# Kernel tuning notes

Measured on AMD Instinct MI355X. Metric: run time of the kernel, lower is better.

The kernel has to match this reference:

```python
import jax, jax.numpy as jnp
import numpy as np

HIDDEN = 1024
INTER = 4096

def setup_inputs() -> dict:
    key = jax.random.key(0)
    k1, k2, k3, k4, k5 = jax.random.split(key, 5)
    hidden_states = jax.random.normal(k1, (4, 2048, HIDDEN), dtype=jnp.float32)
    # Linear params: W stored pre-transposed as [in, out], matching W = dense.weight.t()
    W1 = jax.random.normal(k2, (HIDDEN, INTER), dtype=jnp.float32) * (1.0 / np.sqrt(HIDDEN))
    b1 = jax.random.normal(k3, (INTER,), dtype=jnp.float32) * 0.02
    W2 = jax.random.normal(k4, (INTER, HIDDEN), dtype=jnp.float32) * (1.0 / np.sqrt(INTER))
    b2 = jax.random.normal(k5, (HIDDEN,), dtype=jnp.float32) * 0.02
    return {"hidden_states": hidden_states, "W1": W1, "b1": b1, "W2": W2, "b2": b2}

def reference(hidden_states, W1, b1, W2, b2):
    # Tiled loops in the original are exactly a dense 2-layer MLP with ReLU.
    h = jax.nn.relu(jnp.einsum('bsh,hi->bsi', hidden_states, W1) + b1)
    return jnp.einsum('bsi,ih->bsh', h, W2) + b2
```

## Files before the change

kernel.cpp:

```cpp
#include <hip/hip_runtime.h>
#include <cstddef>

typedef short short8 __attribute__((ext_vector_type(8)));
typedef unsigned short ushort8 __attribute__((ext_vector_type(8)));
typedef float f32x4 __attribute__((ext_vector_type(4)));

#define AS1(p) ((const __attribute__((address_space(1))) void*)(p))
#define AS3(p) ((__attribute__((address_space(3))) void*)(p))

__device__ __forceinline__ unsigned short f2bf(float f) {
  unsigned int u = __builtin_bit_cast(unsigned int, f);
  u += 0x7FFFu + ((u >> 16) & 1u);
  return (unsigned short)(u >> 16);
}

__device__ __forceinline__ void gload_lds16(const void* g, void* l) {
  __builtin_amdgcn_global_load_lds(AS1(g), AS3(l), 16, 0, 0);
}

__global__ void cvt_f32_bf16(const float* __restrict__ in,
                             unsigned short* __restrict__ out, int n4) {
  int i = blockIdx.x * blockDim.x + threadIdx.x;
  if (i >= n4) return;
  float4 v = *reinterpret_cast<const float4*>(in + (size_t)i * 4);
  ushort4 o;
  o.x = f2bf(v.x); o.y = f2bf(v.y); o.z = f2bf(v.z); o.w = f2bf(v.w);
  *reinterpret_cast<ushort4*>(out + (size_t)i * 4) = o;
}

__global__ void transpose_cvt(const float* __restrict__ in,
                              unsigned short* __restrict__ out,
                              int Kd, int Nd) {
  __shared__ float tile[32][33];
  const int n0 = blockIdx.x * 32;
  const int k0 = blockIdx.y * 32;
  const int tx = threadIdx.x;
  const int ty = threadIdx.y;
#pragma unroll
  for (int i = 0; i < 4; ++i)
    tile[ty + i * 8][tx] = in[(size_t)(k0 + ty + i * 8) * Nd + n0 + tx];
  __syncthreads();
#pragma unroll
  for (int i = 0; i < 4; ++i)
    out[(size_t)(n0 + ty + i * 8) * Kd + k0 + tx] = f2bf(tile[tx][ty + i * 8]);
}

template <int A_F32, int RELU_BF16_OUT>
__global__ __launch_bounds__(256, 2)
void gemm_bf16(const void* __restrict__ Ap, int lda,
               const unsigned short* __restrict__ B, int ldb,
               const float* __restrict__ bias,
               void* __restrict__ C, int ldc,
               int K, int beta) {
  __shared__ char lds[32768];
  char* const As = lds;
  char* const Bs = lds + 16384;

  const int tid  = threadIdx.x;
  const int lane = tid & 63;
  const int w    = tid >> 6;
  const int wm   = w >> 1;
  const int wn   = w & 1;
  const int m0   = blockIdx.y * 128;
  const int n0   = blockIdx.x * 128;

  f32x4 acc[4][4];
#pragma unroll
  for (int i = 0; i < 4; ++i)
#pragma unroll
    for (int j = 0; j < 4; ++j)
      acc[i][j] = (f32x4){0.f, 0.f, 0.f, 0.f};

  int srow[4], scol[4], sbase[4];
#pragma unroll
  for (int j = 0; j < 4; ++j) {
    const int stored  = (j * 256 + tid) * 16;
    const int natural = stored ^ (((stored >> 7) & 7) << 4);
    srow[j]  = natural >> 7;
    scol[j]  = (natural & 127) >> 1;
    sbase[j] = (j * 256 + (tid & 192)) * 16;
  }

  size_t agofs[4];
  int ast[4];
  if (A_F32) {
#pragma unroll
    for (int p = 0; p < 4; ++p) {
      const int idx = p * 256 + tid;
      const int r   = idx >> 3;
      const int kbe = (idx & 7) * 8;
      agofs[p] = (size_t)(m0 + r) * lda + kbe;
      const int nat = r * 128 + kbe * 2;
      ast[p] = nat ^ (((nat >> 7) & 7) << 4);
    }
  }

  const int nsteps = K >> 6;
  for (int ks = 0; ks < nsteps; ++ks) {
    const int k0 = ks << 6;
    if (A_F32) {
      const float* Af = (const float*)Ap;
#pragma unroll
      for (int p = 0; p < 4; ++p) {
        const float* s = Af + agofs[p] + k0;
        float4 x0 = *reinterpret_cast<const float4*>(s);
        float4 x1 = *reinterpret_cast<const float4*>(s + 4);
        ushort8 v;
        v[0] = f2bf(x0.x); v[1] = f2bf(x0.y); v[2] = f2bf(x0.z); v[3] = f2bf(x0.w);
        v[4] = f2bf(x1.x); v[5] = f2bf(x1.y); v[6] = f2bf(x1.z); v[7] = f2bf(x1.w);
        *reinterpret_cast<ushort8*>(As + ast[p]) = v;
      }
    } else {
      const unsigned short* Ab = (const unsigned short*)Ap;
#pragma unroll
      for (int j = 0; j < 4; ++j)
        gload_lds16(Ab + (size_t)(m0 + srow[j]) * lda + (k0 + scol[j]),
                    As + sbase[j]);
    }
#pragma unroll
    for (int j = 0; j < 4; ++j)
      gload_lds16(B + (size_t)(n0 + srow[j]) * ldb + (k0 + scol[j]),
                  Bs + sbase[j]);
    __syncthreads();

#pragma unroll
    for (int kk = 0; kk < 2; ++kk) {
      const int kb = kk * 64 + (lane >> 4) * 16;
      short8 af[4], bfv[4];
#pragma unroll
      for (int mi = 0; mi < 4; ++mi) {
        int nat = (wm * 64 + mi * 16 + (lane & 15)) * 128 + kb;
        int st  = nat ^ (((nat >> 7) & 7) << 4);
        af[mi] = *reinterpret_cast<const short8*>(As + st);
      }
#pragma unroll
      for (int ni = 0; ni < 4; ++ni) {
        int nat = (wn * 64 + ni * 16 + (lane & 15)) * 128 + kb;
        int st  = nat ^ (((nat >> 7) & 7) << 4);
        bfv[ni] = *reinterpret_cast<const short8*>(Bs + st);
      }
#pragma unroll
      for (int mi = 0; mi < 4; ++mi)
#pragma unroll
        for (int ni = 0; ni < 4; ++ni)
          acc[mi][ni] = __builtin_amdgcn_mfma_f32_16x16x32_bf16(
              af[mi], bfv[ni], acc[mi][ni], 0, 0, 0);
    }
    __syncthreads();
  }

  const int row0 = m0 + wm * 64 + (lane >> 4) * 4;
  const int col0 = n0 + wn * 64 + (lane & 15);
#pragma unroll
  for (int ni = 0; ni < 4; ++ni) {
    const int c = col0 + ni * 16;
    const float bv = beta ? 0.f : bias[c];
#pragma unroll
    for (int mi = 0; mi < 4; ++mi) {
#pragma unroll
      for (int r = 0; r < 4; ++r) {
        const size_t idx = (size_t)(row0 + mi * 16 + r) * ldc + c;
        float v = acc[mi][ni][r] + bv;
        if (RELU_BF16_OUT) {
          v = v > 0.f ? v : 0.f;
          ((unsigned short*)C)[idx] = f2bf(v);
        } else {
          if (beta) v += ((float*)C)[idx];
          ((float*)C)[idx] = v;
        }
      }
    }
  }
}

extern "C" void kernel_launch(void* const* d_in, const int* in_sizes, int n_in,
                              void* d_out, int out_size, void* d_ws, size_t ws_size,
                              hipStream_t stream) {
  const float* X  = (const float*)d_in[0];
  const float* W1 = (const float*)d_in[1];
  const float* b1 = (const float*)d_in[2];
  const float* W2 = (const float*)d_in[3];
  const float* b2 = (const float*)d_in[4];
  float* out = (float*)d_out;

  const int M = 8192, H = 1024, I = 4096;
  const size_t MB = 1024 * 1024;

  char* ws = (char*)d_ws;
  unsigned short* W1t = (unsigned short*)ws;
  unsigned short* W2t = (unsigned short*)(ws + 8 * MB);

  int Ic;
  int useXbf;
  unsigned short* Xbf = nullptr;
  unsigned short* Hc;
  if (ws_size >= 80 * MB) {
    Ic = 4096; useXbf = 1;
    Xbf = (unsigned short*)((char*)d_out + 16 * MB);
    Hc  = (unsigned short*)(ws + 16 * MB);
  } else if (ws_size >= 64 * MB) {
    Ic = 2048; useXbf = 1;
    Xbf = (unsigned short*)(ws + 16 * MB);
    Hc  = (unsigned short*)(ws + 32 * MB);
  } else if (ws_size >= 48 * MB) {
    Ic = 1024; useXbf = 1;
    Xbf = (unsigned short*)(ws + 16 * MB);
    Hc  = (unsigned short*)(ws + 32 * MB);
  } else if (ws_size >= 32 * MB) {
    Ic = 1024; useXbf = 0;
    Hc  = (unsigned short*)(ws + 16 * MB);
  } else if (ws_size >= 24 * MB) {
    Ic = 512;  useXbf = 0;
    Hc  = (unsigned short*)(ws + 16 * MB);
  } else if (ws_size >= 20 * MB) {
    Ic = 256;  useXbf = 0;
    Hc  = (unsigned short*)(ws + 16 * MB);
  } else {
    Ic = 128;  useXbf = 0;
    Hc  = (unsigned short*)(ws + 16 * MB);
  }

  transpose_cvt<<<dim3(I / 32, H / 32), dim3(32, 8), 0, stream>>>(W1, W1t, H, I);
  transpose_cvt<<<dim3(H / 32, I / 32), dim3(32, 8), 0, stream>>>(W2, W2t, I, H);
  if (useXbf) {
    int n4 = (M * H) / 4;
    cvt_f32_bf16<<<(n4 + 255) / 256, 256, 0, stream>>>(X, Xbf, n4);
  }

  const int nch = I / Ic;
  for (int c = 0; c < nch; ++c) {
    const int i0 = c * Ic;
    if (useXbf)
      gemm_bf16<0, 1><<<dim3(Ic / 128, M / 128), 256, 0, stream>>>(
          Xbf, H, W1t + (size_t)i0 * H, H, b1 + i0, Hc, Ic, H, 0);
    else
      gemm_bf16<1, 1><<<dim3(Ic / 128, M / 128), 256, 0, stream>>>(
          X, H, W1t + (size_t)i0 * H, H, b1 + i0, Hc, Ic, H, 0);
    gemm_bf16<0, 0><<<dim3(H / 128, M / 128), 256, 0, stream>>>(
        Hc, Ic, W2t + i0, I, b2, out, H, Ic, c > 0);
  }
}
```

Before: 168.4 us.

## Add 256-row double-buffered 8-wave GEMM with XCD-aware block remap

Adds a new GEMM kernel with 512 threads and 256xBN tiles. It double-buffers A and B in LDS over 128-wide K steps and splits each step into eight phases, so global-to-LDS loads overlap MFMA work. Barriers, explicit waitcnts and setprio are placed by hand, and block IDs are remapped across the eight XCDs. When the workspace is large, both GEMMs now use this kernel, which aims at higher MFMA utilisation and better reuse. The cost is 128 KB of LDS, which limits occupancy, and fragile hand-tuned synchronisation.

```diff
diff --git a/kernel.cpp b/kernel.cpp
--- a/kernel.cpp
+++ b/kernel.cpp
@@ -43,6 +43,162 @@
 #pragma unroll
   for (int i = 0; i < 4; ++i)
     out[(size_t)(n0 + ty + i * 8) * Kd + k0 + tx] = f2bf(tile[tx][ty + i * 8]);
+}
+
+#define PH(ABUF, BBUF, H, KK, STAGE, WAITC)                                    \
+  {                                                                            \
+    if ((H) == 0) {                                                            \
+      _Pragma("unroll")                                                        \
+      for (int ni = 0; ni < NB; ++ni)                                          \
+        bfr[ni] = *reinterpret_cast<const short8*>((BBUF) + bread[ni][KK]);    \
+    }                                                                          \
+    short8 afr[4];                                                             \
+    _Pragma("unroll")                                                          \
+    for (int m2 = 0; m2 < 4; ++m2)                                             \
+      afr[m2] = *reinterpret_cast<const short8*>((ABUF) + aread[(H)*4+m2][KK]);\
+    STAGE;                                                                     \
+    __builtin_amdgcn_s_barrier();                                              \
+    asm volatile("s_waitcnt lgkmcnt(0)" ::: "memory");                         \
+    __builtin_amdgcn_sched_barrier(0);                                         \
+    __builtin_amdgcn_s_setprio(1);                                             \
+    _Pragma("unroll")                                                          \
+    for (int m2 = 0; m2 < 4; ++m2) {                                           \
+      _Pragma("unroll")                                                        \
+      for (int ni = 0; ni < NB; ++ni)                                          \
+        acc[(H)*4+m2][ni] = __builtin_amdgcn_mfma_f32_16x16x32_bf16(           \
+            afr[m2], bfr[ni], acc[(H)*4+m2][ni], 0, 0, 0);                     \
+    }                                                                          \
+    __builtin_amdgcn_s_setprio(0);                                             \
+    WAITC;                                                                     \
+    __builtin_amdgcn_s_barrier();                                              \
+  }
+
+template <int BN, int RELU_BF16_OUT>
+__global__ __launch_bounds__(512, 2)
+void gemm8p(const unsigned short* __restrict__ A, int lda,
+            const unsigned short* __restrict__ Bp, int ldb,
+            const float* __restrict__ bias,
+            void* __restrict__ C, int ldc, int K, int nbx) {
+  constexpr int PWN     = BN / 4;
+  constexpr int NB      = PWN / 16;
+  constexpr int LOADS_B = BN / 128;
+  constexpr int BHROWS  = BN / 2;
+  constexpr int BHSZ    = BHROWS * 128;
+  extern __shared__ char lds[];
+  char* const A0b = lds;
+  char* const A1b = lds + 32768;
+  char* const B0b = lds + 65536;
+  char* const B1b = lds + 65536 + 2 * BHSZ;
+
+  const int tid  = threadIdx.x;
+  const int lane = tid & 63;
+  const int wid  = tid >> 6;
+  const int wm   = wid >> 2;
+  const int wn   = wid & 3;
+
+  const int cpx     = gridDim.x >> 3;
+  const int logical = (blockIdx.x & 7) * cpx + (blockIdx.x >> 3);
+  const int bx = logical % nbx;
+  const int by = logical / nbx;
+  const int m0 = by * 256;
+  const int n0 = bx * BN;
+
+  f32x4 acc[8][NB];
+#pragma unroll
+  for (int i = 0; i < 8; ++i)
+#pragma unroll
+    for (int j = 0; j < NB; ++j)
+      acc[i][j] = (f32x4){0.f, 0.f, 0.f, 0.f};
+
+  size_t aofs0, aofs1, bofs0, bofs1 = 0;
+  {
+    int sr = tid * 16, nat = sr ^ (((sr >> 7) & 7) << 4);
+    aofs0 = (size_t)(m0 + (nat >> 7)) * lda + ((nat & 127) >> 1);
+    bofs0 = (size_t)(n0 + (nat >> 7)) * ldb + ((nat & 127) >> 1);
+    sr = (512 + tid) * 16; nat = sr ^ (((sr >> 7) & 7) << 4);
+    aofs1 = (size_t)(m0 + (nat >> 7)) * lda + ((nat & 127) >> 1);
+    if (LOADS_B == 2)
+      bofs1 = (size_t)(n0 + (nat >> 7)) * ldb + ((nat & 127) >> 1);
+  }
+  const int dst0 = (tid & 448) * 16;
+  const int dst1 = dst0 + 8192;
+
+  auto stA = [&](char* ab, int half, int kel) {
+    gload_lds16(A + aofs0 + (size_t)half * 128 * lda + kel, ab + half * 16384 + dst0);
+    gload_lds16(A + aofs1 + (size_t)half * 128 * lda + kel, ab + half * 16384 + dst1);
+  };
+  auto stB = [&](char* bb, int half, int kel) {
+    gload_lds16(Bp + bofs0 + (size_t)half * BHROWS * ldb + kel, bb + half * BHSZ + dst0);
+    if constexpr (LOADS_B == 2)
+      gload_lds16(Bp + bofs1 + (size_t)half * BHROWS * ldb + kel, bb + half * BHSZ + dst1);
+  };
+  auto waitLB = [&]() {
+    if constexpr (LOADS_B == 2) asm volatile("s_waitcnt vmcnt(2)" ::: "memory");
+    else                        asm volatile("s_waitcnt vmcnt(1)" ::: "memory");
+  };
+
+  int aread[8][2], bread[NB][2];
+#pragma unroll
+  for (int mi = 0; mi < 8; ++mi)
+#pragma unroll
+    for (int kk = 0; kk < 2; ++kk) {
+      int nat = (wm * 128 + mi * 16 + (lane & 15)) * 128 + kk * 64 + (lane >> 4) * 16;
+      aread[mi][kk] = nat ^ (((nat >> 7) & 7) << 4);
+    }
+#pragma unroll
+  for (int ni = 0; ni < NB; ++ni)
+#pragma unroll
+    for (int kk = 0; kk < 2; ++kk) {
+      int nat = (wn * PWN + ni * 16 + (lane & 15)) * 128 + kk * 64 + (lane >> 4) * 16;
+      bread[ni][kk] = nat ^ (((nat >> 7) & 7) << 4);
+    }
+
+  stB(B0b, 0, 0);
+  stB(B0b, 1, 0);
+  stA(A0b, 0, 0);
+  stA(A0b, 1, 0);
+  stB(B1b, 0, 64);
+  waitLB();
+  __builtin_amdgcn_s_barrier();
+
+  const int niter = K >> 7;
+  for (int it = 0; it < niter; ++it) {
+    const bool last = (it == niter - 1);
+    const int kb = it << 7;
+    short8 bfr[NB];
+    PH(A0b, B0b, 0, 0, stB(B1b, 1, kb + 64), ((void)0));
+    PH(A0b, B0b, 1, 0, stA(A1b, 0, kb + 64), ((void)0));
+    PH(A0b, B0b, 0, 1, stA(A1b, 1, kb + 64), ((void)0));
+    PH(A0b, B0b, 1, 1, { if (!last) stB(B0b, 0, kb + 128); },
+       { if (last) { asm volatile("s_waitcnt vmcnt(0)" ::: "memory"); } else waitLB(); });
+    PH(A1b, B1b, 0, 0, { if (!last) stB(B0b, 1, kb + 128); }, ((void)0));
+    PH(A1b, B1b, 1, 0, { if (!last) stA(A0b, 0, kb + 128); }, ((void)0));
+    PH(A1b, B1b, 0, 1, { if (!last) stA(A0b, 1, kb + 128); }, ((void)0));
+    PH(A1b, B1b, 1, 1, { if (!last) stB(B1b, 0, kb + 192); },
+       { if (!last) waitLB(); });
+  }
+
+  const int row0 = m0 + wm * 128 + (lane >> 4) * 4;
+  const int col0 = n0 + wn * PWN + (lane & 15);
+#pragma unroll
+  for (int ni = 0; ni < NB; ++ni) {
+    const int c = col0 + ni * 16;
+    const float bv = bias[c];
+#pragma unroll
+    for (int mi = 0; mi < 8; ++mi) {
+#pragma unroll
+      for (int r = 0; r < 4; ++r) {
+        const size_t idx = (size_t)(row0 + mi * 16 + r) * ldc + c;
+        float v = acc[mi][ni][r] + bv;
+        if (RELU_BF16_OUT) {
+          v = v > 0.f ? v : 0.f;
+          ((unsigned short*)C)[idx] = f2bf(v);
+        } else {
+          ((float*)C)[idx] = v;
+        }
+      }
+    }
+  }
 }
 
 template <int A_F32, int RELU_BF16_OUT>
@@ -190,15 +346,23 @@
   unsigned short* W1t = (unsigned short*)ws;
   unsigned short* W2t = (unsigned short*)(ws + 8 * MB);
 
-  int Ic;
-  int useXbf;
+  transpose_cvt<<<dim3(I / 32, H / 32), dim3(32, 8), 0, stream>>>(W1, W1t, H, I);
+  transpose_cvt<<<dim3(H / 32, I / 32), dim3(32, 8), 0, stream>>>(W2, W2t, I, H);
+
+  if (ws_size >= 80 * MB) {
+    unsigned short* Xbf = (unsigned short*)((char*)d_out + 16 * MB);
+    unsigned short* Hbf = (unsigned short*)(ws + 16 * MB);
+    int n4 = (M * H) / 4;
+    cvt_f32_bf16<<<(n4 + 255) / 256, 256, 0, stream>>>(X, Xbf, n4);
+    gemm8p<256, 1><<<512, 512, 131072, stream>>>(Xbf, H, W1t, H, b1, Hbf, I, H, I / 256);
+    gemm8p<128, 0><<<256, 512, 98304, stream>>>(Hbf, I, W2t, I, b2, out, H, I, H / 128);
+    return;
+  }
+
+  int Ic, useXbf;
   unsigned short* Xbf = nullptr;
   unsigned short* Hc;
-  if (ws_size >= 80 * MB) {
-    Ic = 4096; useXbf = 1;
-    Xbf = (unsigned short*)((char*)d_out + 16 * MB);
-    Hc  = (unsigned short*)(ws + 16 * MB);
-  } else if (ws_size >= 64 * MB) {
+  if (ws_size >= 64 * MB) {
     Ic = 2048; useXbf = 1;
     Xbf = (unsigned short*)(ws + 16 * MB);
     Hc  = (unsigned short*)(ws + 32 * MB);
@@ -220,8 +384,6 @@
     Hc  = (unsigned short*)(ws + 16 * MB);
   }
 
-  transpose_cvt<<<dim3(I / 32, H / 32), dim3(32, 8), 0, stream>>>(W1, W1t, H, I);
-  transpose_cvt<<<dim3(H / 32, I / 32), dim3(32, 8), 0, stream>>>(W2, W2t, I, H);
   if (useXbf) {
     int n4 = (M * H) / 4;
     cvt_f32_bf16<<<(n4 + 255) / 256, 256, 0, stream>>>(X, Xbf, n4);
```

Result: no change. 165.4 us (-1.7%).

## Add 4-stage LDS ring-buffered 256-row GEMM kernel for large-workspace path

Applied to the files above, without the earlier changes.

Introduces a new gemm_ring kernel with 512 threads and 256xBN tiles. It uses a 4-slot LDS ring filled by direct global-to-LDS loads three k-steps ahead, with explicit vmcnt waits, sched barriers and setprio around the MFMA blocks. It also remaps block IDs into XCD-grouped order and uses a new XOR swizzle. The large-workspace path now runs both GEMMs with this kernel, which aims to hide memory latency and raise MFMA utilisation. In exchange it uses much more LDS and registers, and the hand-coded wait counts must match the issue order exactly.

```diff
diff --git a/kernel.cpp b/kernel.cpp
--- a/kernel.cpp
+++ b/kernel.cpp
@@ -16,6 +16,11 @@
 
 __device__ __forceinline__ void gload_lds16(const void* g, void* l) {
   __builtin_amdgcn_global_load_lds(AS1(g), AS3(l), 16, 0, 0);
+}
+
+template <int N>
+__device__ __forceinline__ void vwait() {
+  asm volatile("s_waitcnt vmcnt(%0)" :: "n"(N) : "memory");
 }
 
 __global__ void cvt_f32_bf16(const float* __restrict__ in,
@@ -43,6 +48,146 @@
 #pragma unroll
   for (int i = 0; i < 4; ++i)
     out[(size_t)(n0 + ty + i * 8) * Kd + k0 + tx] = f2bf(tile[tx][ty + i * 8]);
+}
+
+#define TILE_BODY(T, DO_STAGE, STAGE_T)                                        \
+  {                                                                            \
+    char* s = lds + (size_t)((T) & 3) * SLOT;                                  \
+    _Pragma("unroll")                                                          \
+    for (int h = 0; h < NPH; ++h) {                                            \
+      if (h == 0) {                                                            \
+        _Pragma("unroll")                                                      \
+        for (int ni = 0; ni < 4; ++ni)                                         \
+          bfr[ni] = *reinterpret_cast<const short8*>(s + brd[ni]);             \
+      }                                                                        \
+      short8 afr[4];                                                           \
+      _Pragma("unroll")                                                        \
+      for (int m2 = 0; m2 < 4; ++m2)                                           \
+        afr[m2] = *reinterpret_cast<const short8*>(s + ard[h * 4 + m2]);       \
+      if (h == 0 && (DO_STAGE)) stage(STAGE_T);                                \
+      asm volatile("s_waitcnt lgkmcnt(0)" ::: "memory");                       \
+      __builtin_amdgcn_sched_barrier(0);                                       \
+      __builtin_amdgcn_s_setprio(1);                                           \
+      _Pragma("unroll")                                                        \
+      for (int m2 = 0; m2 < 4; ++m2) {                                         \
+        _Pragma("unroll")                                                      \
+        for (int ni = 0; ni < 4; ++ni)                                         \
+          acc[h * 4 + m2][ni] = __builtin_amdgcn_mfma_f32_16x16x32_bf16(       \
+              afr[m2], bfr[ni], acc[h * 4 + m2][ni], 0, 0, 0);                 \
+      }                                                                        \
+      __builtin_amdgcn_s_setprio(0);                                           \
+    }                                                                          \
+  }
+
+#define TILE_END(WN_)                                                          \
+  vwait<WN_>();                                                                \
+  __builtin_amdgcn_s_barrier();                                                \
+  __builtin_amdgcn_sched_barrier(0);
+
+template <int WM, int BN, int RELU_BF16_OUT>
+__global__ __launch_bounds__(512, 2)
+void gemm_ring(const unsigned short* __restrict__ A, int lda,
+               const unsigned short* __restrict__ B, int ldb,
+               const float* __restrict__ bias,
+               void* __restrict__ C, int ldc, int K, int nbx) {
+  constexpr int WN     = 8 / WM;
+  constexpr int MB     = 256 / WM / 16;
+  constexpr int NPH    = MB / 4;
+  constexpr int BUNITS = BN / 128;
+  constexpr int UNITS  = 2 + BUNITS;
+  constexpr int SLOT   = 16384 + BN * 64;
+  extern __shared__ char lds[];
+
+  const int tid  = threadIdx.x;
+  const int lane = tid & 63;
+  const int wid  = tid >> 6;
+  const int wm   = wid / WN;
+  const int wn   = wid % WN;
+
+  const int cpx     = gridDim.x >> 3;
+  const int logical = (blockIdx.x & 7) * cpx + (blockIdx.x >> 3);
+  const int bx = logical % nbx;
+  const int by = logical / nbx;
+  const int m0 = by * 256;
+  const int n0 = bx * BN;
+
+  f32x4 acc[MB][4];
+#pragma unroll
+  for (int i = 0; i < MB; ++i)
+#pragma unroll
+    for (int j = 0; j < 4; ++j)
+      acc[i][j] = (f32x4){0.f, 0.f, 0.f, 0.f};
+
+  const int p    = tid * 16;
+  const int r    = p >> 6;
+  const int smsk = (((r & 3) ^ ((r >> 2) & 3)) << 4);
+  const int kel0 = (((p & 63) ^ smsk) >> 1);
+  size_t aofs0 = (size_t)(m0 + r) * lda + kel0;
+  size_t aofs1 = (size_t)(m0 + 128 + r) * lda + kel0;
+  size_t bofs0 = (size_t)(n0 + r) * ldb + kel0;
+  size_t bofs1 = (BUNITS == 2) ? (size_t)(n0 + 128 + r) * ldb + kel0 : 0;
+  const int ldst = (tid >> 6) * 1024;
+
+  auto stage = [&](int t) {
+    char* s = lds + (size_t)(t & 3) * SLOT;
+    const int kk = t * 32;
+    gload_lds16(A + aofs0 + kk, s + ldst);
+    gload_lds16(A + aofs1 + kk, s + 8192 + ldst);
+    gload_lds16(B + bofs0 + kk, s + 16384 + ldst);
+    if constexpr (BUNITS == 2)
+      gload_lds16(B + bofs1 + kk, s + 24576 + ldst);
+  };
+
+  int ard[MB], brd[4];
+#pragma unroll
+  for (int mi = 0; mi < MB; ++mi) {
+    int nat = (wm * (MB * 16) + mi * 16 + (lane & 15)) * 64 + (lane >> 4) * 16;
+    int rr  = nat >> 6;
+    ard[mi] = nat ^ ((((rr & 3) ^ ((rr >> 2) & 3))) << 4);
+  }
+#pragma unroll
+  for (int ni = 0; ni < 4; ++ni) {
+    int nat = (wn * 64 + ni * 16 + (lane & 15)) * 64 + (lane >> 4) * 16;
+    int rr  = nat >> 6;
+    brd[ni] = 16384 + (nat ^ ((((rr & 3) ^ ((rr >> 2) & 3))) << 4));
+  }
+
+  stage(0); stage(1); stage(2);
+  TILE_END(2 * UNITS);
+
+  const int NT = K >> 5;
+  short8 bfr[4];
+  for (int t = 0; t < NT - 3; ++t) {
+    TILE_BODY(t, true, t + 3);
+    TILE_END(2 * UNITS);
+  }
+  TILE_BODY(NT - 3, false, 0);
+  TILE_END(UNITS);
+  TILE_BODY(NT - 2, false, 0);
+  TILE_END(0);
+  TILE_BODY(NT - 1, false, 0);
+
+  const int row0 = m0 + wm * (MB * 16) + (lane >> 4) * 4;
+  const int col0 = n0 + wn * 64 + (lane & 15);
+#pragma unroll
+  for (int ni = 0; ni < 4; ++ni) {
+    const int c = col0 + ni * 16;
+    const float bv = bias[c];
+#pragma unroll
+    for (int mi = 0; mi < MB; ++mi) {
+#pragma unroll
+      for (int rr = 0; rr < 4; ++rr) {
+        const size_t idx = (size_t)(row0 + mi * 16 + rr) * ldc + c;
+        float v = acc[mi][ni][rr] + bv;
+        if (RELU_BF16_OUT) {
+          v = v > 0.f ? v : 0.f;
+          ((unsigned short*)C)[idx] = f2bf(v);
+        } else {
+          ((float*)C)[idx] = v;
+        }
+      }
+    }
+  }
 }
 
 template <int A_F32, int RELU_BF16_OUT>
@@ -85,13 +230,13 @@
   int ast[4];
   if (A_F32) {
 #pragma unroll
-    for (int p = 0; p < 4; ++p) {
-      const int idx = p * 256 + tid;
-      const int r   = idx >> 3;
+    for (int pq = 0; pq < 4; ++pq) {
+      const int idx = pq * 256 + tid;
+      const int rr  = idx >> 3;
       const int kbe = (idx & 7) * 8;
-      agofs[p] = (size_t)(m0 + r) * lda + kbe;
-      const int nat = r * 128 + kbe * 2;
-      ast[p] = nat ^ (((nat >> 7) & 7) << 4);
+      agofs[pq] = (size_t)(m0 + rr) * lda + kbe;
+      const int nat = rr * 128 + kbe * 2;
+      ast[pq] = nat ^ (((nat >> 7) & 7) << 4);
     }
   }
 
@@ -101,14 +246,14 @@
     if (A_F32) {
       const float* Af = (const float*)Ap;
 #pragma unroll
-      for (int p = 0; p < 4; ++p) {
-        const float* s = Af + agofs[p] + k0;
-        float4 x0 = *reinterpret_cast<const float4*>(s);
-        float4 x1 = *reinterpret_cast<const float4*>(s + 4);
+      for (int pq = 0; pq < 4; ++pq) {
+        const float* sp = Af + agofs[pq] + k0;
+        float4 x0 = *reinterpret_cast<const float4*>(sp);
+        float4 x1 = *reinterpret_cast<const float4*>(sp + 4);
         ushort8 v;
         v[0] = f2bf(x0.x); v[1] = f2bf(x0.y); v[2] = f2bf(x0.z); v[3] = f2bf(x0.w);
         v[4] = f2bf(x1.x); v[5] = f2bf(x1.y); v[6] = f2bf(x1.z); v[7] = f2bf(x1.w);
-        *reinterpret_cast<ushort8*>(As + ast[p]) = v;
+        *reinterpret_cast<ushort8*>(As + ast[pq]) = v;
       }
     } else {
       const unsigned short* Ab = (const unsigned short*)Ap;
@@ -158,9 +303,9 @@
 #pragma unroll
     for (int mi = 0; mi < 4; ++mi) {
 #pragma unroll
-      for (int r = 0; r < 4; ++r) {
-        const size_t idx = (size_t)(row0 + mi * 16 + r) * ldc + c;
-        float v = acc[mi][ni][r] + bv;
+      for (int rr = 0; rr < 4; ++rr) {
+        const size_t idx = (size_t)(row0 + mi * 16 + rr) * ldc + c;
+        float v = acc[mi][ni][rr] + bv;
         if (RELU_BF16_OUT) {
           v = v > 0.f ? v : 0.f;
           ((unsigned short*)C)[idx] = f2bf(v);
@@ -190,15 +335,25 @@
   unsigned short* W1t = (unsigned short*)ws;
   unsigned short* W2t = (unsigned short*)(ws + 8 * MB);
 
-  int Ic;
-  int useXbf;
+  transpose_cvt<<<dim3(I / 32, H / 32), dim3(32, 8), 0, stream>>>(W1, W1t, H, I);
+  transpose_cvt<<<dim3(H / 32, I / 32), dim3(32, 8), 0, stream>>>(W2, W2t, I, H);
+
+  if (ws_size >= 80 * MB) {
+    unsigned short* Xbf = (unsigned short*)((char*)d_out + 16 * MB);
+    unsigned short* Hbf = (unsigned short*)(ws + 16 * MB);
+    int n4 = (M * H) / 4;
+    cvt_f32_bf16<<<(n4 + 255) / 256, 256, 0, stream>>>(X, Xbf, n4);
+    gemm_ring<2, 256, 1><<<512, 512, 131072, stream>>>(
+        Xbf, H, W1t, H, b1, Hbf, I, H, I / 256);
+    gemm_ring<4, 128, 0><<<256, 512, 98304, stream>>>(
+        Hbf, I, W2t, I, b2, out, H, I, H / 128);
+    return;
+  }
+
+  int Ic, useXbf;
   unsigned short* Xbf = nullptr;
   unsigned short* Hc;
-  if (ws_size >= 80 * MB) {
-    Ic = 4096; useXbf = 1;
-    Xbf = (unsigned short*)((char*)d_out + 16 * MB);
-    Hc  = (unsigned short*)(ws + 16 * MB);
-  } else if (ws_size >= 64 * MB) {
+  if (ws_size >= 64 * MB) {
     Ic = 2048; useXbf = 1;
     Xbf = (unsigned short*)(ws + 16 * MB);
     Hc  = (unsigned short*)(ws + 32 * MB);
@@ -220,8 +375,6 @@
     Hc  = (unsigned short*)(ws + 16 * MB);
   }
 
-  transpose_cvt<<<dim3(I / 32, H / 32), dim3(32, 8), 0, stream>>>(W1, W1t, H, I);
-  transpose_cvt<<<dim3(H / 32, I / 32), dim3(32, 8), 0, stream>>>(W2, W2t, I, H);
   if (useXbf) {
     int n4 = (M * H) / 4;
     cvt_f32_bf16<<<(n4 + 255) / 256, 256, 0, stream>>>(X, Xbf, n4);
```

Result: slower. 172.9 us (+2.7%).

## Use narrower N tile for second GEMM, XCD-aware block remap, raise occupancy

Applied to the files above, without the earlier changes.

Templates the GEMM on the N tile width and uses a 128x64 tile for the second GEMM, which doubles that grid to 1024 blocks and improves load balance across CUs. Blocks are launched on a 1D grid and remapped so consecutive logical tiles land on the same XCD (blockIdx mod 8), aiming at better L2 reuse. Launch bounds rise to 4 waves per SIMD to raise occupancy, which risks register pressure. The narrower tile lowers B reuse per block and adds more A reloads.

```diff
diff --git a/kernel.cpp b/kernel.cpp
--- a/kernel.cpp
+++ b/kernel.cpp
@@ -45,14 +45,16 @@
     out[(size_t)(n0 + ty + i * 8) * Kd + k0 + tx] = f2bf(tile[tx][ty + i * 8]);
 }
 
-template <int A_F32, int RELU_BF16_OUT>
-__global__ __launch_bounds__(256, 2)
+template <int A_F32, int BN, int RELU_BF16_OUT>
+__global__ __launch_bounds__(256, 4)
 void gemm_bf16(const void* __restrict__ Ap, int lda,
                const unsigned short* __restrict__ B, int ldb,
                const float* __restrict__ bias,
                void* __restrict__ C, int ldc,
-               int K, int beta) {
-  __shared__ char lds[32768];
+               int K, int beta, int nbx) {
+  constexpr int BUNITS = BN / 32;
+  constexpr int NB     = BN / 32;
+  __shared__ char lds[16384 + BN * 128];
   char* const As = lds;
   char* const Bs = lds + 16384;
 
@@ -61,14 +63,17 @@
   const int w    = tid >> 6;
   const int wm   = w >> 1;
   const int wn   = w & 1;
-  const int m0   = blockIdx.y * 128;
-  const int n0   = blockIdx.x * 128;
-
-  f32x4 acc[4][4];
+
+  const int cpx     = gridDim.x >> 3;
+  const int logical = (blockIdx.x & 7) * cpx + (blockIdx.x >> 3);
+  const int m0 = (logical / nbx) * 128;
+  const int n0 = (logical % nbx) * BN;
+
+  f32x4 acc[4][NB];
 #pragma unroll
   for (int i = 0; i < 4; ++i)
 #pragma unroll
-    for (int j = 0; j < 4; ++j)
+    for (int j = 0; j < NB; ++j)
       acc[i][j] = (f32x4){0.f, 0.f, 0.f, 0.f};
 
   int srow[4], scol[4], sbase[4];
@@ -118,7 +123,7 @@
                     As + sbase[j]);
     }
 #pragma unroll
-    for (int j = 0; j < 4; ++j)
+    for (int j = 0; j < BUNITS; ++j)
       gload_lds16(B + (size_t)(n0 + srow[j]) * ldb + (k0 + scol[j]),
                   Bs + sbase[j]);
     __syncthreads();
@@ -126,7 +131,7 @@
 #pragma unroll
     for (int kk = 0; kk < 2; ++kk) {
       const int kb = kk * 64 + (lane >> 4) * 16;
-      short8 af[4], bfv[4];
+      short8 af[4], bfv[NB];
 #pragma unroll
       for (int mi = 0; mi < 4; ++mi) {
         int nat = (wm * 64 + mi * 16 + (lane & 15)) * 128 + kb;
@@ -134,15 +139,15 @@
         af[mi] = *reinterpret_cast<const short8*>(As + st);
       }
 #pragma unroll
-      for (int ni = 0; ni < 4; ++ni) {
-        int nat = (wn * 64 + ni * 16 + (lane & 15)) * 128 + kb;
+      for (int ni = 0; ni < NB; ++ni) {
+        int nat = (wn * (BN / 2) + ni * 16 + (lane & 15)) * 128 + kb;
         int st  = nat ^ (((nat >> 7) & 7) << 4);
         bfv[ni] = *reinterpret_cast<const short8*>(Bs + st);
       }
 #pragma unroll
       for (int mi = 0; mi < 4; ++mi)
 #pragma unroll
-        for (int ni = 0; ni < 4; ++ni)
+        for (int ni = 0; ni < NB; ++ni)
           acc[mi][ni] = __builtin_amdgcn_mfma_f32_16x16x32_bf16(
               af[mi], bfv[ni], acc[mi][ni], 0, 0, 0);
     }
@@ -150,9 +155,9 @@
   }
 
   const int row0 = m0 + wm * 64 + (lane >> 4) * 4;
-  const int col0 = n0 + wn * 64 + (lane & 15);
-#pragma unroll
-  for (int ni = 0; ni < 4; ++ni) {
+  const int col0 = n0 + wn * (BN / 2) + (lane & 15);
+#pragma unroll
+  for (int ni = 0; ni < NB; ++ni) {
     const int c = col0 + ni * 16;
     const float bv = beta ? 0.f : bias[c];
 #pragma unroll
@@ -190,15 +195,25 @@
   unsigned short* W1t = (unsigned short*)ws;
   unsigned short* W2t = (unsigned short*)(ws + 8 * MB);
 
-  int Ic;
-  int useXbf;
+  transpose_cvt<<<dim3(I / 32, H / 32), dim3(32, 8), 0, stream>>>(W1, W1t, H, I);
+  transpose_cvt<<<dim3(H / 32, I / 32), dim3(32, 8), 0, stream>>>(W2, W2t, I, H);
+
+  if (ws_size >= 80 * MB) {
+    unsigned short* Xbf = (unsigned short*)((char*)d_out + 16 * MB);
+    unsigned short* Hbf = (unsigned short*)(ws + 16 * MB);
+    int n4 = (M * H) / 4;
+    cvt_f32_bf16<<<(n4 + 255) / 256, 256, 0, stream>>>(X, Xbf, n4);
+    gemm_bf16<0, 128, 1><<<2048, 256, 0, stream>>>(
+        Xbf, H, W1t, H, b1, Hbf, I, H, 0, I / 128);
+    gemm_bf16<0, 64, 0><<<1024, 256, 0, stream>>>(
+        Hbf, I, W2t, I, b2, out, H, I, 0, H / 64);
+    return;
+  }
+
+  int Ic, useXbf;
   unsigned short* Xbf = nullptr;
   unsigned short* Hc;
-  if (ws_size >= 80 * MB) {
-    Ic = 4096; useXbf = 1;
-    Xbf = (unsigned short*)((char*)d_out + 16 * MB);
-    Hc  = (unsigned short*)(ws + 16 * MB);
-  } else if (ws_size >= 64 * MB) {
+  if (ws_size >= 64 * MB) {
     Ic = 2048; useXbf = 1;
     Xbf = (unsigned short*)(ws + 16 * MB);
     Hc  = (unsigned short*)(ws + 32 * MB);
@@ -220,8 +235,6 @@
     Hc  = (unsigned short*)(ws + 16 * MB);
   }
 
-  transpose_cvt<<<dim3(I / 32, H / 32), dim3(32, 8), 0, stream>>>(W1, W1t, H, I);
-  transpose_cvt<<<dim3(H / 32, I / 32), dim3(32, 8), 0, stream>>>(W2, W2t, I, H);
   if (useXbf) {
     int n4 = (M * H) / 4;
     cvt_f32_bf16<<<(n4 + 255) / 256, 256, 0, stream>>>(X, Xbf, n4);
@@ -230,13 +243,14 @@
   const int nch = I / Ic;
   for (int c = 0; c < nch; ++c) {
     const int i0 = c * Ic;
+    const int nbx1 = Ic / 128;
     if (useXbf)
-      gemm_bf16<0, 1><<<dim3(Ic / 128, M / 128), 256, 0, stream>>>(
-          Xbf, H, W1t + (size_t)i0 * H, H, b1 + i0, Hc, Ic, H, 0);
+      gemm_bf16<0, 128, 1><<<nbx1 * (M / 128), 256, 0, stream>>>(
+          Xbf, H, W1t + (size_t)i0 * H, H, b1 + i0, Hc, Ic, H, 0, nbx1);
     else
-      gemm_bf16<1, 1><<<dim3(Ic / 128, M / 128), 256, 0, stream>>>(
-          X, H, W1t + (size_t)i0 * H, H, b1 + i0, Hc, Ic, H, 0);
-    gemm_bf16<0, 0><<<dim3(H / 128, M / 128), 256, 0, stream>>>(
-        Hc, Ic, W2t + i0, I, b2, out, H, Ic, c > 0);
-  }
-}
+      gemm_bf16<1, 128, 1><<<nbx1 * (M / 128), 256, 0, stream>>>(
+          X, H, W1t + (size_t)i0 * H, H, b1 + i0, Hc, Ic, H, 0, nbx1);
+    gemm_bf16<0, 64, 0><<<(H / 64) * (M / 128), 256, 0, stream>>>(
+        Hc, Ic, W2t + i0, I, b2, out, H, Ic, c > 0, H / 64);
+  }
+}
```

After: 176.8 us. 5.0% more time.
